# Kernel optimization log

Hardware: AMD Instinct MI355X
Metric: run time of the kernel (lower is better)

The kernel has to match this reference:

```python
import jax, jax.numpy as jnp
import numpy as np

MUL = 32          # multiplicity of 0e and 1o channels
NRAD = 8          # radial basis size
NPATH = 7         # TP instructions

# Orthonormal symmetric-traceless basis for the real l=2 irrep -> Cartesian map
_B = np.zeros((5, 3, 3))
_s2 = 1.0 / np.sqrt(2.0)
_B[0, 0, 1] = _B[0, 1, 0] = _s2                      # xy
_B[1, 1, 2] = _B[1, 2, 1] = _s2                      # yz
_B[2] = np.diag([-1.0, -1.0, 2.0]) / np.sqrt(6.0)    # 2z^2-x^2-y^2
_B[3, 0, 2] = _B[3, 2, 0] = _s2                      # xz
_B[4] = np.diag([1.0, -1.0, 0.0]) / np.sqrt(2.0)     # x^2-y^2
# w3j(1,2,1)[i,M,k], Frobenius-normalized to 1 (e3nn convention)
C121 = jnp.asarray(np.transpose(_B, (1, 0, 2)) / np.sqrt(5.0), jnp.float32)
INV_SQRT3 = float(1.0 / np.sqrt(3.0))   # w3j(1,1,0) / w3j(0,1,1) / w3j(1,0,1)
A0 = float(1.0 / np.sqrt(64.0))         # path weight, l=0 outs: sqrt(1/fan_in), fan_in=2*32
A1 = float(np.sqrt(3.0 / 96.0))         # path weight, l=1 out: sqrt((2l+1)/fan_in), fan_in=3*32


def setup_inputs() -> dict:
    key = jax.random.key(0)
    ks = jax.random.split(key, 9)
    N, E = 4096, 32768
    x = jax.random.normal(ks[0], (N, 4 * MUL), jnp.float32)
    edge_attr = jax.random.normal(ks[1], (E, 9), jnp.float32)
    edge_length = jax.random.uniform(ks[2], (E,), jnp.float32) * 5.0
    edge_src = jax.random.randint(ks[3], (E,), 0, N)
    edge_dst = jax.random.randint(ks[4], (E,), 0, N)
    W_fc1 = jax.random.normal(ks[5], (NRAD, 64), jnp.float32)
    W_fc2 = jax.random.normal(ks[6], (64, NPATH * MUL * MUL), jnp.float32)
    W_sc_s = jax.random.normal(ks[7], (MUL, MUL), jnp.float32)
    W_sc_v = jax.random.normal(ks[8], (MUL, MUL), jnp.float32)
    return dict(x=x, edge_attr=edge_attr, edge_length=edge_length,
                edge_src=edge_src, edge_dst=edge_dst,
                W_fc1=W_fc1, W_fc2=W_fc2, W_sc_s=W_sc_s, W_sc_v=W_sc_v)


def reference(x, edge_attr, edge_length, edge_src, edge_dst, W_fc1, W_fc2, W_sc_s, W_sc_v):
    N = x.shape[0]
    # radial Gaussian basis: centers linspace(0,5,8), sigma = spacing
    centers = jnp.linspace(0.0, 5.0, NRAD)
    sigma = 5.0 / (NRAD - 1)
    d = edge_length[:, None] - centers[None, :]
    radial = jnp.exp(-d * d / (2.0 * sigma * sigma))
    # radial MLP -> per-edge TP weights (e3nn FullyConnectedNet: W/sqrt(fan_in), silu)
    h = jax.nn.silu(radial @ (W_fc1 / jnp.sqrt(jnp.float32(NRAD))))
    w = h @ (W_fc2 / jnp.sqrt(jnp.float32(64)))          # [E, 7168]
    W = w.reshape(-1, NPATH, MUL, MUL)                    # [E,7,u,w]
    # split node features: 32x0e scalars + 32x1o vectors
    s = x[:, :MUL]
    v = x[:, MUL:].reshape(N, MUL, 3)
    sj = s[edge_src]                                      # [E,u]
    vj = v[edge_src]                                      # [E,u,3]
    y0 = edge_attr[:, 0]
    y1 = edge_attr[:, 1:4]
    y2 = edge_attr[:, 4:9]
    # tensor-product paths
    t00 = sj * y0[:, None]                                            # 0e x 0e
    t11 = jnp.einsum('eui,ei->eu', vj, y1) * INV_SQRT3                # 1o x 1o -> 0e
    out_s = (jnp.einsum('eu,euw->ew', t00, W[:, 0]) +
             jnp.einsum('eu,euw->ew', t11, W[:, 1])) * A0             # scalars
    out_g = (jnp.einsum('eu,euw->ew', t00, W[:, 2]) +
             jnp.einsum('eu,euw->ew', t11, W[:, 3])) * A0             # gates
    t01 = sj[:, :, None] * y1[:, None, :] * INV_SQRT3                 # 0e x 1o -> 1o
    t10 = vj * (y0[:, None, None] * INV_SQRT3)                        # 1o x 0e -> 1o
    t12 = jnp.einsum('eui,imk,em->euk', vj, C121, y2)                 # 1o x 2e -> 1o
    out_v = (jnp.einsum('euk,euw->ewk', t01, W[:, 4]) +
             jnp.einsum('euk,euw->ewk', t10, W[:, 5]) +
             jnp.einsum('euk,euw->ewk', t12, W[:, 6])) * A1           # [E,w,3]
    m_ij = jnp.concatenate([out_s, out_g, out_v.reshape(-1, 3 * MUL)], axis=1)  # [E,160]
    # scatter-mean over destination nodes
    sums = jax.ops.segment_sum(m_ij, edge_dst, num_segments=N)
    cnt = jax.ops.segment_sum(jnp.ones((m_ij.shape[0],), m_ij.dtype), edge_dst, num_segments=N)
    m_i = sums / jnp.clip(cnt, 1.0)[:, None]
    # gate: silu on scalars, sigmoid gates multiply the 1o block per-channel
    gs = jax.nn.silu(m_i[:, :MUL])
    gate = jax.nn.sigmoid(m_i[:, MUL:2 * MUL])
    gv = m_i[:, 2 * MUL:].reshape(N, MUL, 3) * gate[:, :, None]
    # residual self-connection (e3nn o3.Linear: per-irrep, / sqrt(mul_in))
    inv_sqrt_mul = 1.0 / jnp.sqrt(jnp.float32(MUL))
    h_s = gs + (s @ W_sc_s) * inv_sqrt_mul
    h_v = gv + jnp.einsum('nui,uw->nwi', v, W_sc_v) * inv_sqrt_mul
    # o3.Norm: per-irrep L2 norm over the (2l+1) components
    norm_s = jnp.sqrt(h_s * h_s + 1e-12)
    norm_v = jnp.sqrt(jnp.sum(h_v * h_v, axis=-1) + 1e-12)
    return jnp.concatenate([norm_s, norm_v], axis=1)       # [N, 64]
```

## Files before the change

kernel.cpp:

```cpp
#include <hip/hip_runtime.h>

#define NIVL  256
#define KINV  51.2f
#define KSTEP 0.01953125f
#define TPW   7168
#define BCAP  256
#define DCAP  64
#define NROW  11
#define TSTR  40
#define PREPT 455

typedef __attribute__((ext_vector_type(8))) __bf16 bf16x8;
typedef __attribute__((ext_vector_type(4))) float f32x4;
union FragU { uint4 u; bf16x8 v; };

__device__ __forceinline__ float sigmoidf_(float v) { return 1.f / (1.f + expf(-v)); }
__device__ __forceinline__ unsigned bf16r_(float x) { return (__float_as_uint(x) + 0x8000u) >> 16; }
__device__ __forceinline__ unsigned pk_(float lo, float hi) { return (bf16r_(hi) << 16) | bf16r_(lo); }

__device__ __forceinline__ f32x4 mfma_(bf16x8 a, bf16x8 b, f32x4 c) {
    return __builtin_amdgcn_mfma_f32_16x16x32_bf16(a, b, c, 0, 0, 0);
}

__global__ __launch_bounds__(256)
void prep_kernel(const float* __restrict__ W1, const float* __restrict__ W2,
                 const float* __restrict__ elen, const int* __restrict__ esrc,
                 const int* __restrict__ edst, const float* __restrict__ ea,
                 float* __restrict__ T, int* __restrict__ cntL, int* __restrict__ cntD,
                 float* __restrict__ erec, int* __restrict__ sortedD, int E)
{
    const int tid = threadIdx.x;
    if (blockIdx.x < PREPT) {
        __shared__ float hk_s[4][64];
        const int bx = blockIdx.x % 7;
        const int k0 = (blockIdx.x / 7) * 4;
        const int pw = bx * 1024 + tid * 4;
        {
            int kk = tid >> 6, c = tid & 63;
            float L = (float)(k0 + kk) * KSTEP;
            float d = 0.f;
#pragma unroll
            for (int r = 0; r < 8; ++r) {
                float dd = L - (float)r * (5.f / 7.f);
                d += expf(-dd * dd * 0.98f) * W1[r * 64 + c];
            }
            d *= 0.3535533906f;
            hk_s[kk][c] = d * sigmoidf_(d) * 0.125f;
        }
        __syncthreads();
        float4 acc[4];
#pragma unroll
        for (int q = 0; q < 4; ++q) acc[q] = make_float4(0.f, 0.f, 0.f, 0.f);
#pragma unroll 4
        for (int c = 0; c < 64; ++c) {
            float4 w4 = *(const float4*)(W2 + (size_t)c * TPW + pw);
#pragma unroll
            for (int q = 0; q < 4; ++q) {
                float hv = hk_s[q][c];
                acc[q].x = fmaf(hv, w4.x, acc[q].x);
                acc[q].y = fmaf(hv, w4.y, acc[q].y);
                acc[q].z = fmaf(hv, w4.z, acc[q].z);
                acc[q].w = fmaf(hv, w4.w, acc[q].w);
            }
        }
#pragma unroll
        for (int q = 0; q < 4; ++q) {
            int k = k0 + q;
            if (k < 257)
                *(float4*)(T + (size_t)k * TPW + pw) = acc[q];
        }
    } else {
        const float I3 = 0.5773502692f, I5 = 0.4472135955f, S2 = 0.7071067812f;
        const float I6 = 0.4082482905f, T6 = 0.8164965809f;
        int e = (blockIdx.x - PREPT) * 256 + tid;
        if (e < E) {
            float t = elen[e] * KINV;
            int j = (int)t; j = j > 255 ? 255 : j;
            int pos = atomicAdd(&cntL[j], 1);
            if (pos < BCAP) {
                const float* y = ea + (size_t)e * 9;
                float y0 = y[0];
                float a = y[4], b = y[5], c = y[6], d2 = y[7], ee = y[8];
                float4 r0, r1, r2, r3;
                r0.x = t - (float)j;
                r0.y = __int_as_float(esrc[e]);
                r0.z = __int_as_float(e);
                r0.w = y0;
                r1.x = y0 * I3;
                r1.y = y[1] * I3; r1.z = y[2] * I3; r1.w = y[3] * I3;
                r2.x = (-c * I6 + ee * S2) * I5;
                r2.y = a * S2 * I5;
                r2.z = d2 * S2 * I5;
                r2.w = (-c * I6 - ee * S2) * I5;
                r3.x = b * S2 * I5;
                r3.y = c * T6 * I5;
                r3.z = 0.f; r3.w = 0.f;
                float4* dst = (float4*)(erec + ((size_t)j * BCAP + pos) * 16);
                dst[0] = r0; dst[1] = r1; dst[2] = r2; dst[3] = r3;
            }
            int d = edst[e];
            int pd = atomicAdd(&cntD[d], 1);
            if (pd < DCAP) sortedD[d * DCAP + pd] = e;
        }
    }
}

__global__ __launch_bounds__(256, 2)
void fold_kernel(const float* __restrict__ x, const int* __restrict__ cntL,
                 const float* __restrict__ erec, const float* __restrict__ T,
                 float* __restrict__ msg)
{
    const int j = blockIdx.x >> 1, half = blockIdx.x & 1;
    __shared__ uint4 BF[7 * 2 * 2 * 64];
    __shared__ __align__(16) unsigned short TB[2 * NROW * 16 * TSTR];
    __shared__ float ECF[32];
    __shared__ int   ECE[32];
    const int tid = threadIdx.x;

    const int cnt = min(cntL[j], BCAP);
    const int nchunk = (cnt + 31) >> 5;
    const int te = tid & 31, sub = tid >> 5;

    float4 er0 = {0,0,0,0}, er1 = {0,0,0,0}, er2 = {0,0,0,0}, er3 = {0,0,0,0};
    if (half < nchunk) {
        int ce = min(32, cnt - (half << 5));
        if (te < ce) {
            const float4* rp = (const float4*)(erec + ((size_t)j * BCAP + (half << 5) + te) * 16);
            er0 = rp[0]; er1 = rp[1]; er2 = rp[2]; er3 = rp[3];
        }
    }

    const float* Trow  = T + (size_t)j * TPW;
    const float* Trow2 = Trow + TPW;
    for (int i = tid; i < 896; i += 256) {
        int pl = i >> 7, rem = i & 127;
        int whs = rem >> 6, lane_s = rem & 63;
        int u0 = (lane_s >> 4) * 8, w = whs * 16 + (lane_s & 15);
        int basei = pl * 1024 + w;
        unsigned ta[4], dd[4];
#pragma unroll
        for (int q = 0; q < 4; ++q) {
            float a0 = Trow[basei + (u0 + 2 * q) * 32];
            float a1 = Trow[basei + (u0 + 2 * q + 1) * 32];
            float b0 = Trow2[basei + (u0 + 2 * q) * 32];
            float b1 = Trow2[basei + (u0 + 2 * q + 1) * 32];
            ta[q] = pk_(a0, a1);
            dd[q] = pk_(b0 - a0, b1 - a1);
        }
        BF[(pl * 4 + whs) * 64 + lane_s]     = make_uint4(ta[0], ta[1], ta[2], ta[3]);
        BF[(pl * 4 + 2 + whs) * 64 + lane_s] = make_uint4(dd[0], dd[1], dd[2], dd[3]);
    }

    const int wv = tid >> 6, lane = tid & 63;
    const int sg = wv >> 1, wh = wv & 1;
    const int col = lane & 15, quad = lane >> 4;
    const float A0 = 0.125f, A1 = 0.1767766953f;

    for (int ci = half; ci < nchunk; ci += 2) {
        const int base = ci << 5;
        const int cntE = min(32, cnt - base);

        const int u0 = sub * 4;
        float s4[4], vv[12];
        if (te < cntE) {
            int src = __float_as_int(er0.y);
            const float* xp = x + (size_t)src * 128;
            *(float4*)s4 = *(const float4*)(xp + u0);
            *(float4*)(vv)     = *(const float4*)(xp + 32 + 3 * u0);
            *(float4*)(vv + 4) = *(const float4*)(xp + 32 + 3 * u0 + 4);
            *(float4*)(vv + 8) = *(const float4*)(xp + 32 + 3 * u0 + 8);
        }
        float4 nr0 = {0,0,0,0}, nr1 = {0,0,0,0}, nr2 = {0,0,0,0}, nr3 = {0,0,0,0};
        const int cin = ci + 2;
        if (cin < nchunk) {
            int ce2 = min(32, cnt - (cin << 5));
            if (te < ce2) {
                const float4* rp = (const float4*)(erec + ((size_t)j * BCAP + (cin << 5) + te) * 16);
                nr0 = rp[0]; nr1 = rp[1]; nr2 = rp[2]; nr3 = rp[3];
            }
        }

        __syncthreads();

        {
            const int esg = te >> 4, e16 = te & 15;
            float rv[NROW][4];
            if (te < cntE) {
                float y0 = er0.w;
                float y0i = er1.x, y1i0 = er1.y, y1i1 = er1.z, y1i2 = er1.w;
                float M0 = er2.x, M1 = er2.y, M2 = er2.z, M4 = er2.w;
                float M5 = er3.x, M8 = er3.y;
                if (sub == 0) {
                    ECF[te] = er0.x;
                    ECE[te] = __float_as_int(er0.z);
                }
#pragma unroll
                for (int up = 0; up < 4; ++up) {
                    float s = s4[up];
                    float v0 = vv[3 * up], v1 = vv[3 * up + 1], v2 = vv[3 * up + 2];
                    rv[0][up] = s * y0;
                    rv[1][up] = v0 * y1i0 + v1 * y1i1 + v2 * y1i2;
                    rv[2][up] = s * y1i0;
                    rv[3][up] = s * y1i1;
                    rv[4][up] = s * y1i2;
                    rv[5][up] = v0 * y0i;
                    rv[6][up] = v1 * y0i;
                    rv[7][up] = v2 * y0i;
                    rv[8][up]  = v0 * M0 + v1 * M1 + v2 * M2;
                    rv[9][up]  = v0 * M1 + v1 * M4 + v2 * M5;
                    rv[10][up] = v0 * M2 + v1 * M5 + v2 * M8;
                }
            } else {
#pragma unroll
                for (int r = 0; r < NROW; ++r)
#pragma unroll
                    for (int up = 0; up < 4; ++up) rv[r][up] = 0.f;
            }
#pragma unroll
            for (int r = 0; r < NROW; ++r) {
                unsigned lo = pk_(rv[r][0], rv[r][1]);
                unsigned hi = pk_(rv[r][2], rv[r][3]);
                *(uint2*)&TB[((esg * NROW + r) * 16 + e16) * TSTR + u0] = make_uint2(lo, hi);
            }
        }
        __syncthreads();

        f32x4 cS0 = {0,0,0,0}, cS1 = {0,0,0,0}, cG0 = {0,0,0,0}, cG1 = {0,0,0,0};
        f32x4 cV[3][2];
#pragma unroll
        for (int k = 0; k < 3; ++k) { cV[k][0] = (f32x4){0,0,0,0}; cV[k][1] = (f32x4){0,0,0,0}; }

        #define LOADA(r) ({ FragU fa_; fa_.u = *(const uint4*)&TB[((sg * NROW + (r)) * 16 + col) * TSTR + quad * 8]; fa_.v; })
        #define LOADB(p, tad) ({ FragU fb_; fb_.u = BF[((p) * 4 + (tad) * 2 + wh) * 64 + lane]; fb_.v; })

        bf16x8 a0 = LOADA(0), a1 = LOADA(1);
        cS0 = mfma_(a0, LOADB(0, 0), cS0); cS0 = mfma_(a1, LOADB(1, 0), cS0);
        cS1 = mfma_(a0, LOADB(0, 1), cS1); cS1 = mfma_(a1, LOADB(1, 1), cS1);
        cG0 = mfma_(a0, LOADB(2, 0), cG0); cG0 = mfma_(a1, LOADB(3, 0), cG0);
        cG1 = mfma_(a0, LOADB(2, 1), cG1); cG1 = mfma_(a1, LOADB(3, 1), cG1);
#pragma unroll
        for (int k = 0; k < 3; ++k) {
            bf16x8 ak;
            ak = LOADA(2 + k);
            cV[k][0] = mfma_(ak, LOADB(4, 0), cV[k][0]);
            cV[k][1] = mfma_(ak, LOADB(4, 1), cV[k][1]);
            ak = LOADA(5 + k);
            cV[k][0] = mfma_(ak, LOADB(5, 0), cV[k][0]);
            cV[k][1] = mfma_(ak, LOADB(5, 1), cV[k][1]);
            ak = LOADA(8 + k);
            cV[k][0] = mfma_(ak, LOADB(6, 0), cV[k][0]);
            cV[k][1] = mfma_(ak, LOADB(6, 1), cV[k][1]);
        }

        const int w = wh * 16 + col;
#pragma unroll
        for (int reg = 0; reg < 4; ++reg) {
            int e = sg * 16 + quad * 4 + reg;
            if (e < cntE) {
                float f = ECF[e];
                int eid = ECE[e];
                float* mp = msg + (size_t)eid * 160;
                mp[w]            = (cS0[reg] + f * cS1[reg]) * A0;
                mp[32 + w]       = (cG0[reg] + f * cG1[reg]) * A0;
                mp[64 + 3 * w]     = (cV[0][0][reg] + f * cV[0][1][reg]) * A1;
                mp[64 + 3 * w + 1] = (cV[1][0][reg] + f * cV[1][1][reg]) * A1;
                mp[64 + 3 * w + 2] = (cV[2][0][reg] + f * cV[2][1][reg]) * A1;
            }
        }
        #undef LOADA
        #undef LOADB
        er0 = nr0; er1 = nr1; er2 = nr2; er3 = nr3;
    }
}

__global__ __launch_bounds__(256)
void node_kernel(const float* __restrict__ x, const float* __restrict__ Wss,
                 const float* __restrict__ Wsv, const float* __restrict__ msg,
                 const int* __restrict__ sortedD, const int* __restrict__ cntD,
                 float* __restrict__ out, int N)
{
    __shared__ float ms[8][160];
    const int tid = threadIdx.x;
    const int n0 = blockIdx.x * 8;
    const float IM = 0.1767766953f;

#pragma unroll
    for (int it = 0; it < 5; ++it) {
        int task = tid + it * 256;
        int nl = task / 160;
        int c = task - nl * 160;
        int n = n0 + nl;
        if (n < N) {
            int cd = cntD[n];
            int cc = cd < DCAP ? cd : DCAP;
            const int* sp = sortedD + n * DCAP;
            float s = 0.f;
            for (int i0 = 0; i0 < cc; i0 += 8) {
                int4 ia = *(const int4*)(sp + i0);
                int4 ib = *(const int4*)(sp + i0 + 4);
                int id[8] = { ia.x, ia.y, ia.z, ia.w, ib.x, ib.y, ib.z, ib.w };
                float p[8];
#pragma unroll
                for (int k = 0; k < 8; ++k)
                    p[k] = (i0 + k < cc) ? msg[(size_t)id[k] * 160 + c] : 0.f;
#pragma unroll
                for (int k = 0; k < 8; ++k) s += p[k];
            }
            ms[nl][c] = s / fmaxf((float)cd, 1.f);
        }
    }
    __syncthreads();

#pragma unroll
    for (int it = 0; it < 2; ++it) {
        int task = tid + it * 256;
        int nl = task >> 6, col = task & 63;
        int n = n0 + nl;
        if (n >= N) continue;
        const float* m  = ms[nl];
        const float* xp = x + (size_t)n * 128;
        if (col < 32) {
            int w = col;
            float mval = m[w];
            float gs = mval * sigmoidf_(mval);
            float dot = 0.f;
#pragma unroll 4
            for (int u = 0; u < 32; ++u) dot += xp[u] * Wss[u * 32 + w];
            float hs = gs + dot * IM;
            out[(size_t)n * 64 + w] = sqrtf(hs * hs + 1e-12f);
        } else {
            int w = col - 32;
            float gate = sigmoidf_(m[32 + w]);
            float g0 = m[64 + 3 * w + 0] * gate;
            float g1 = m[64 + 3 * w + 1] * gate;
            float g2 = m[64 + 3 * w + 2] * gate;
            float d0 = 0.f, d1 = 0.f, d2 = 0.f;
#pragma unroll 4
            for (int u = 0; u < 32; ++u) {
                float wv = Wsv[u * 32 + w];
                d0 += xp[32 + 3 * u + 0] * wv;
                d1 += xp[32 + 3 * u + 1] * wv;
                d2 += xp[32 + 3 * u + 2] * wv;
            }
            float h0 = g0 + d0 * IM, h1 = g1 + d1 * IM, h2 = g2 + d2 * IM;
            out[(size_t)n * 64 + 32 + w] = sqrtf(h0 * h0 + h1 * h1 + h2 * h2 + 1e-12f);
        }
    }
}

extern "C" void kernel_launch(void* const* d_in, const int* in_sizes, int n_in,
                              void* d_out, int out_size, void* d_ws, size_t ws_size,
                              hipStream_t stream)
{
    const float* x    = (const float*)d_in[0];
    const float* ea   = (const float*)d_in[1];
    const float* elen = (const float*)d_in[2];
    const int*   esrc = (const int*)d_in[3];
    const int*   edst = (const int*)d_in[4];
    const float* W1   = (const float*)d_in[5];
    const float* W2   = (const float*)d_in[6];
    const float* Wss  = (const float*)d_in[7];
    const float* Wsv  = (const float*)d_in[8];
    float* out = (float*)d_out;

    const int N = in_sizes[0] / 128;
    const int E = in_sizes[2];

    float* T      = (float*)d_ws;
    float* msg    = T + (size_t)257 * TPW;
    float* erec   = msg + (size_t)E * 160;
    int*   cntL   = (int*)(erec + (size_t)256 * BCAP * 16);
    int*   cntD   = cntL + 256;
    int*   sortedD= cntD + N;

    hipMemsetAsync(cntL, 0, (size_t)(256 + N) * sizeof(int), stream);

    prep_kernel<<<PREPT + (E + 255) / 256, 256, 0, stream>>>(W1, W2, elen, esrc, edst, ea, T, cntL, cntD, erec, sortedD, E);
    fold_kernel<<<NIVL * 2, 256, 0, stream>>>(x, cntL, erec, T, msg);
    node_kernel<<<(N + 7) / 8, 256, 0, stream>>>(x, Wss, Wsv, msg, sortedD, cntD, out, N);
}
```

Before: 138.6 us.

## Scatter edge messages via float atomics into per-node sums instead of msg buffer

Edge messages are no longer written to a per-edge [E,160] buffer that node_kernel later gathers through a sorted destination list. The fold kernel now atomically adds each message into a per-node sums array keyed by the destination stored in the edge record, and node_kernel just divides by the count. This removes the large intermediate write and the gather traffic, and it also drops the DCAP cap on edges per node. The cost is a larger memset, float atomic contention, and nondeterministic summation order.

Result: slower. 156.5 us (+12.9%).

```diff
diff --git a/kernel.cpp b/kernel.cpp
--- a/kernel.cpp
+++ b/kernel.cpp
@@ -5,7 +5,6 @@
 #define KSTEP 0.01953125f
 #define TPW   7168
 #define BCAP  256
-#define DCAP  64
 #define NROW  11
 #define TSTR  40
 #define PREPT 455
@@ -27,7 +26,7 @@
                  const float* __restrict__ elen, const int* __restrict__ esrc,
                  const int* __restrict__ edst, const float* __restrict__ ea,
                  float* __restrict__ T, int* __restrict__ cntL, int* __restrict__ cntD,
-                 float* __restrict__ erec, int* __restrict__ sortedD, int E)
+                 float* __restrict__ erec, int E)
 {
     const int tid = threadIdx.x;
     if (blockIdx.x < PREPT) {
@@ -76,6 +75,7 @@
         if (e < E) {
             float t = elen[e] * KINV;
             int j = (int)t; j = j > 255 ? 255 : j;
+            int d = edst[e];
             int pos = atomicAdd(&cntL[j], 1);
             if (pos < BCAP) {
                 const float* y = ea + (size_t)e * 9;
@@ -84,7 +84,7 @@
                 float4 r0, r1, r2, r3;
                 r0.x = t - (float)j;
                 r0.y = __int_as_float(esrc[e]);
-                r0.z = __int_as_float(e);
+                r0.z = __int_as_float(d);
                 r0.w = y0;
                 r1.x = y0 * I3;
                 r1.y = y[1] * I3; r1.z = y[2] * I3; r1.w = y[3] * I3;
@@ -98,9 +98,7 @@
                 float4* dst = (float4*)(erec + ((size_t)j * BCAP + pos) * 16);
                 dst[0] = r0; dst[1] = r1; dst[2] = r2; dst[3] = r3;
             }
-            int d = edst[e];
-            int pd = atomicAdd(&cntD[d], 1);
-            if (pd < DCAP) sortedD[d * DCAP + pd] = e;
+            atomicAdd(&cntD[d], 1);
         }
     }
 }
@@ -108,7 +106,7 @@
 __global__ __launch_bounds__(256, 2)
 void fold_kernel(const float* __restrict__ x, const int* __restrict__ cntL,
                  const float* __restrict__ erec, const float* __restrict__ T,
-                 float* __restrict__ msg)
+                 float* __restrict__ sums)
 {
     const int j = blockIdx.x >> 1, half = blockIdx.x & 1;
     __shared__ uint4 BF[7 * 2 * 2 * 64];
@@ -258,13 +256,13 @@
             int e = sg * 16 + quad * 4 + reg;
             if (e < cntE) {
                 float f = ECF[e];
-                int eid = ECE[e];
-                float* mp = msg + (size_t)eid * 160;
-                mp[w]            = (cS0[reg] + f * cS1[reg]) * A0;
-                mp[32 + w]       = (cG0[reg] + f * cG1[reg]) * A0;
-                mp[64 + 3 * w]     = (cV[0][0][reg] + f * cV[0][1][reg]) * A1;
-                mp[64 + 3 * w + 1] = (cV[1][0][reg] + f * cV[1][1][reg]) * A1;
-                mp[64 + 3 * w + 2] = (cV[2][0][reg] + f * cV[2][1][reg]) * A1;
+                int dst = ECE[e];
+                float* mp = sums + (size_t)dst * 160;
+                unsafeAtomicAdd(mp + w,              (cS0[reg] + f * cS1[reg]) * A0);
+                unsafeAtomicAdd(mp + 32 + w,         (cG0[reg] + f * cG1[reg]) * A0);
+                unsafeAtomicAdd(mp + 64 + 3 * w,     (cV[0][0][reg] + f * cV[0][1][reg]) * A1);
+                unsafeAtomicAdd(mp + 64 + 3 * w + 1, (cV[1][0][reg] + f * cV[1][1][reg]) * A1);
+                unsafeAtomicAdd(mp + 64 + 3 * w + 2, (cV[2][0][reg] + f * cV[2][1][reg]) * A1);
             }
         }
         #undef LOADA
@@ -275,9 +273,8 @@
 
 __global__ __launch_bounds__(256)
 void node_kernel(const float* __restrict__ x, const float* __restrict__ Wss,
-                 const float* __restrict__ Wsv, const float* __restrict__ msg,
-                 const int* __restrict__ sortedD, const int* __restrict__ cntD,
-                 float* __restrict__ out, int N)
+                 const float* __restrict__ Wsv, const float* __restrict__ sums,
+                 const int* __restrict__ cntD, float* __restrict__ out, int N)
 {
     __shared__ float ms[8][160];
     const int tid = threadIdx.x;
@@ -285,28 +282,19 @@
     const float IM = 0.1767766953f;
 
 #pragma unroll
-    for (int it = 0; it < 5; ++it) {
+    for (int it = 0; it < 2; ++it) {
         int task = tid + it * 256;
-        int nl = task / 160;
-        int c = task - nl * 160;
-        int n = n0 + nl;
-        if (n < N) {
-            int cd = cntD[n];
-            int cc = cd < DCAP ? cd : DCAP;
-            const int* sp = sortedD + n * DCAP;
-            float s = 0.f;
-            for (int i0 = 0; i0 < cc; i0 += 8) {
-                int4 ia = *(const int4*)(sp + i0);
-                int4 ib = *(const int4*)(sp + i0 + 4);
-                int id[8] = { ia.x, ia.y, ia.z, ia.w, ib.x, ib.y, ib.z, ib.w };
-                float p[8];
-#pragma unroll
-                for (int k = 0; k < 8; ++k)
-                    p[k] = (i0 + k < cc) ? msg[(size_t)id[k] * 160 + c] : 0.f;
-#pragma unroll
-                for (int k = 0; k < 8; ++k) s += p[k];
-            }
-            ms[nl][c] = s / fmaxf((float)cd, 1.f);
+        if (task < 320) {
+            int nl = task / 40, q = task - nl * 40;
+            int n = n0 + nl;
+            if (n < N) {
+                float inv = 1.f / fmaxf((float)cntD[n], 1.f);
+                float4 v = *(const float4*)(sums + (size_t)n * 160 + q * 4);
+                ms[nl][q * 4 + 0] = v.x * inv;
+                ms[nl][q * 4 + 1] = v.y * inv;
+                ms[nl][q * 4 + 2] = v.z * inv;
+                ms[nl][q * 4 + 3] = v.w * inv;
+            }
         }
     }
     __syncthreads();
@@ -367,15 +355,14 @@
     const int E = in_sizes[2];
 
     float* T      = (float*)d_ws;
-    float* msg    = T + (size_t)257 * TPW;
-    float* erec   = msg + (size_t)E * 160;
-    int*   cntL   = (int*)(erec + (size_t)256 * BCAP * 16);
+    float* erec   = T + (size_t)257 * TPW;
+    float* sums   = erec + (size_t)256 * BCAP * 16;
+    int*   cntL   = (int*)(sums + (size_t)N * 160);
     int*   cntD   = cntL + 256;
-    int*   sortedD= cntD + N;
-
-    hipMemsetAsync(cntL, 0, (size_t)(256 + N) * sizeof(int), stream);
-
-    prep_kernel<<<PREPT + (E + 255) / 256, 256, 0, stream>>>(W1, W2, elen, esrc, edst, ea, T, cntL, cntD, erec, sortedD, E);
-    fold_kernel<<<NIVL * 2, 256, 0, stream>>>(x, cntL, erec, T, msg);
-    node_kernel<<<(N + 7) / 8, 256, 0, stream>>>(x, Wss, Wsv, msg, sortedD, cntD, out, N);
-}
+
+    hipMemsetAsync(sums, 0, ((size_t)N * 160 + 256 + N) * sizeof(float), stream);
+
+    prep_kernel<<<PREPT + (E + 255) / 256, 256, 0, stream>>>(W1, W2, elen, esrc, edst, ea, T, cntL, cntD, erec, E);
+    fold_kernel<<<NIVL * 2, 256, 0, stream>>>(x, cntL, erec, T, sums);
+    node_kernel<<<(N + 7) / 8, 256, 0, stream>>>(x, Wss, Wsv, sums, cntD, out, N);
+}
```

## Keep TP weight fragments in registers and split fold work across four blocks

Applied to the files above, without the earlier changes.

Removes the shared-memory BF staging of bf16 weight fragments. Each lane now builds its own 14 B fragments in registers straight from the T rows. The grid goes from 2 to 4 blocks per interval, striding chunks by 4, with occupancy hint raised to 3 blocks per CU. This cuts LDS use and a sync, and adds parallelism for the fold step, but each block redundantly reloads the T weights from global memory, and the register-held fragments raise VGPR pressure.

Measured after the change: 149.8 us. 1.08x slower.

```diff
diff --git a/kernel.cpp b/kernel.cpp
--- a/kernel.cpp
+++ b/kernel.cpp
@@ -105,13 +105,12 @@
     }
 }
 
-__global__ __launch_bounds__(256, 2)
+__global__ __launch_bounds__(256, 3)
 void fold_kernel(const float* __restrict__ x, const int* __restrict__ cntL,
                  const float* __restrict__ erec, const float* __restrict__ T,
                  float* __restrict__ msg)
 {
-    const int j = blockIdx.x >> 1, half = blockIdx.x & 1;
-    __shared__ uint4 BF[7 * 2 * 2 * 64];
+    const int j = blockIdx.x >> 2, qtr = blockIdx.x & 3;
     __shared__ __align__(16) unsigned short TB[2 * NROW * 16 * TSTR];
     __shared__ float ECF[32];
     __shared__ int   ECE[32];
@@ -120,43 +119,44 @@
     const int cnt = min(cntL[j], BCAP);
     const int nchunk = (cnt + 31) >> 5;
     const int te = tid & 31, sub = tid >> 5;
-
-    float4 er0 = {0,0,0,0}, er1 = {0,0,0,0}, er2 = {0,0,0,0}, er3 = {0,0,0,0};
-    if (half < nchunk) {
-        int ce = min(32, cnt - (half << 5));
-        if (te < ce) {
-            const float4* rp = (const float4*)(erec + ((size_t)j * BCAP + (half << 5) + te) * 16);
-            er0 = rp[0]; er1 = rp[1]; er2 = rp[2]; er3 = rp[3];
-        }
-    }
-
-    const float* Trow  = T + (size_t)j * TPW;
-    const float* Trow2 = Trow + TPW;
-    for (int i = tid; i < 896; i += 256) {
-        int pl = i >> 7, rem = i & 127;
-        int whs = rem >> 6, lane_s = rem & 63;
-        int u0 = (lane_s >> 4) * 8, w = whs * 16 + (lane_s & 15);
-        int basei = pl * 1024 + w;
-        unsigned ta[4], dd[4];
-#pragma unroll
-        for (int q = 0; q < 4; ++q) {
-            float a0 = Trow[basei + (u0 + 2 * q) * 32];
-            float a1 = Trow[basei + (u0 + 2 * q + 1) * 32];
-            float b0 = Trow2[basei + (u0 + 2 * q) * 32];
-            float b1 = Trow2[basei + (u0 + 2 * q + 1) * 32];
-            ta[q] = pk_(a0, a1);
-            dd[q] = pk_(b0 - a0, b1 - a1);
-        }
-        BF[(pl * 4 + whs) * 64 + lane_s]     = make_uint4(ta[0], ta[1], ta[2], ta[3]);
-        BF[(pl * 4 + 2 + whs) * 64 + lane_s] = make_uint4(dd[0], dd[1], dd[2], dd[3]);
-    }
-
     const int wv = tid >> 6, lane = tid & 63;
     const int sg = wv >> 1, wh = wv & 1;
     const int col = lane & 15, quad = lane >> 4;
+
+    float4 er0 = {0,0,0,0}, er1 = {0,0,0,0}, er2 = {0,0,0,0}, er3 = {0,0,0,0};
+    if (qtr < nchunk) {
+        int ce = min(32, cnt - (qtr << 5));
+        if (te < ce) {
+            const float4* rp = (const float4*)(erec + ((size_t)j * BCAP + (qtr << 5) + te) * 16);
+            er0 = rp[0]; er1 = rp[1]; er2 = rp[2]; er3 = rp[3];
+        }
+    }
+
+    bf16x8 Bt[7][2];
+    {
+        const float* Trow  = T + (size_t)j * TPW;
+        const float* Trow2 = Trow + TPW;
+        const int u0 = quad * 8, w = wh * 16 + col;
+#pragma unroll
+        for (int pl = 0; pl < 7; ++pl) {
+            unsigned ta[4], dd[4];
+#pragma unroll
+            for (int q = 0; q < 4; ++q) {
+                float a0 = Trow[pl * 1024 + (u0 + 2 * q) * 32 + w];
+                float a1 = Trow[pl * 1024 + (u0 + 2 * q + 1) * 32 + w];
+                float b0 = Trow2[pl * 1024 + (u0 + 2 * q) * 32 + w];
+                float b1 = Trow2[pl * 1024 + (u0 + 2 * q + 1) * 32 + w];
+                ta[q] = pk_(a0, a1);
+                dd[q] = pk_(b0 - a0, b1 - a1);
+            }
+            FragU fa; fa.u = make_uint4(ta[0], ta[1], ta[2], ta[3]); Bt[pl][0] = fa.v;
+            FragU fd; fd.u = make_uint4(dd[0], dd[1], dd[2], dd[3]); Bt[pl][1] = fd.v;
+        }
+    }
+
     const float A0 = 0.125f, A1 = 0.1767766953f;
 
-    for (int ci = half; ci < nchunk; ci += 2) {
+    for (int ci = qtr; ci < nchunk; ci += 4) {
         const int base = ci << 5;
         const int cntE = min(32, cnt - base);
 
@@ -171,7 +171,7 @@
             *(float4*)(vv + 8) = *(const float4*)(xp + 32 + 3 * u0 + 8);
         }
         float4 nr0 = {0,0,0,0}, nr1 = {0,0,0,0}, nr2 = {0,0,0,0}, nr3 = {0,0,0,0};
-        const int cin = ci + 2;
+        const int cin = ci + 4;
         if (cin < nchunk) {
             int ce2 = min(32, cnt - (cin << 5));
             if (te < ce2) {
@@ -231,25 +231,24 @@
         for (int k = 0; k < 3; ++k) { cV[k][0] = (f32x4){0,0,0,0}; cV[k][1] = (f32x4){0,0,0,0}; }
 
         #define LOADA(r) ({ FragU fa_; fa_.u = *(const uint4*)&TB[((sg * NROW + (r)) * 16 + col) * TSTR + quad * 8]; fa_.v; })
-        #define LOADB(p, tad) ({ FragU fb_; fb_.u = BF[((p) * 4 + (tad) * 2 + wh) * 64 + lane]; fb_.v; })
 
         bf16x8 a0 = LOADA(0), a1 = LOADA(1);
-        cS0 = mfma_(a0, LOADB(0, 0), cS0); cS0 = mfma_(a1, LOADB(1, 0), cS0);
-        cS1 = mfma_(a0, LOADB(0, 1), cS1); cS1 = mfma_(a1, LOADB(1, 1), cS1);
-        cG0 = mfma_(a0, LOADB(2, 0), cG0); cG0 = mfma_(a1, LOADB(3, 0), cG0);
-        cG1 = mfma_(a0, LOADB(2, 1), cG1); cG1 = mfma_(a1, LOADB(3, 1), cG1);
+        cS0 = mfma_(a0, Bt[0][0], cS0); cS0 = mfma_(a1, Bt[1][0], cS0);
+        cS1 = mfma_(a0, Bt[0][1], cS1); cS1 = mfma_(a1, Bt[1][1], cS1);
+        cG0 = mfma_(a0, Bt[2][0], cG0); cG0 = mfma_(a1, Bt[3][0], cG0);
+        cG1 = mfma_(a0, Bt[2][1], cG1); cG1 = mfma_(a1, Bt[3][1], cG1);
 #pragma unroll
         for (int k = 0; k < 3; ++k) {
             bf16x8 ak;
             ak = LOADA(2 + k);
-            cV[k][0] = mfma_(ak, LOADB(4, 0), cV[k][0]);
-            cV[k][1] = mfma_(ak, LOADB(4, 1), cV[k][1]);
+            cV[k][0] = mfma_(ak, Bt[4][0], cV[k][0]);
+            cV[k][1] = mfma_(ak, Bt[4][1], cV[k][1]);
             ak = LOADA(5 + k);
-            cV[k][0] = mfma_(ak, LOADB(5, 0), cV[k][0]);
-            cV[k][1] = mfma_(ak, LOADB(5, 1), cV[k][1]);
+            cV[k][0] = mfma_(ak, Bt[5][0], cV[k][0]);
+            cV[k][1] = mfma_(ak, Bt[5][1], cV[k][1]);
             ak = LOADA(8 + k);
-            cV[k][0] = mfma_(ak, LOADB(6, 0), cV[k][0]);
-            cV[k][1] = mfma_(ak, LOADB(6, 1), cV[k][1]);
+            cV[k][0] = mfma_(ak, Bt[6][0], cV[k][0]);
+            cV[k][1] = mfma_(ak, Bt[6][1], cV[k][1]);
         }
 
         const int w = wh * 16 + col;
@@ -268,7 +267,6 @@
             }
         }
         #undef LOADA
-        #undef LOADB
         er0 = nr0; er1 = nr1; er2 = nr2; er3 = nr3;
     }
 }
@@ -376,6 +374,6 @@
     hipMemsetAsync(cntL, 0, (size_t)(256 + N) * sizeof(int), stream);
 
     prep_kernel<<<PREPT + (E + 255) / 256, 256, 0, stream>>>(W1, W2, elen, esrc, edst, ea, T, cntL, cntD, erec, sortedD, E);
-    fold_kernel<<<NIVL * 2, 256, 0, stream>>>(x, cntL, erec, T, msg);
+    fold_kernel<<<NIVL * 4, 256, 0, stream>>>(x, cntL, erec, T, msg);
     node_kernel<<<(N + 7) / 8, 256, 0, stream>>>(x, Wss, Wsv, msg, sortedD, cntD, out, N);
 }
```
